# Performance work log

Hardware: AMD Instinct MI355X
Metric: run time of the kernel (lower is better)

Reference implementation:

```python
import jax, jax.numpy as jnp
import numpy as np
import math

N, D, BITS = 2048, 1024, 8
K = 1 << BITS          # 256 centroids
NG = (D + 1) // 2      # 512 rotation groups

def setup_inputs() -> dict:
    key = jax.random.key(0)
    kx, kc, kr = jax.random.split(key, 3)
    x = jax.random.normal(kx, (N, D), dtype=jnp.float32)
    # Lloyd-Max style scalar codebook: sorted centroids for a Gaussian source
    centroids = jnp.sort(jax.random.normal(kc, (K,), dtype=jnp.float32))
    # random planar rotations: [cos(theta), sin(theta)] per 2D group
    angles = jax.random.uniform(kr, (NG,), dtype=jnp.float32) * (2.0 * math.pi)
    rot2 = jnp.stack([jnp.cos(angles), jnp.sin(angles)], axis=-1)  # [NG, 2]
    return {"x": x, "centroids": centroids, "rot2": rot2}

def reference(x, centroids, rot2):
    d = x.shape[-1]
    n_groups = rot2.shape[0]
    d_padded = 2 * n_groups
    # unit-normalize rows
    norms = jnp.clip(jnp.linalg.norm(x, axis=-1, keepdims=True), 1e-8)  # [N,1]
    x_unit = x / norms
    pad = d_padded - d
    if pad > 0:
        x_unit = jnp.pad(x_unit, [(0, 0)] * (x.ndim - 1) + [(0, pad)])
    v = x_unit.reshape(*x.shape[:-1], n_groups, 2)                      # [N,NG,2]
    c, s = rot2[..., 0], rot2[..., 1]
    v0, v1 = v[..., 0], v[..., 1]
    v_rot = jnp.stack([c * v0 - s * v1, s * v0 + c * v1], axis=-1)      # rotate
    flat = v_rot.reshape(*v_rot.shape[:-2], -1)                         # [N,d_padded]
    # per-scalar nearest-centroid quantization
    indices = jnp.argmin(jnp.abs(flat[..., None] - centroids), axis=-1) # [N,d_padded]
    values = centroids[indices]
    v_q = values.reshape(*values.shape[:-1], n_groups, 2)
    q0, q1 = v_q[..., 0], v_q[..., 1]
    v_rec = jnp.stack([c * q0 + s * q1, -s * q0 + c * q1], axis=-1)     # inverse rotate
    x_hat = v_rec.reshape(*v_rec.shape[:-2], -1)[..., :d] * norms       # rescale
    return (x_hat, indices)
```

## Files before the change

kernel.cpp:

```cpp
#include <hip/hip_runtime.h>
#include <cfloat>

#define NROWS 2048
#define DDIM  1024
#define KCEN  256

__global__ __launch_bounds__(256)
void planar_quant_kernel(const float* __restrict__ x,
                         const float* __restrict__ cen,
                         const float* __restrict__ rot,
                         float* __restrict__ out_xhat,
                         float* __restrict__ out_idx)
{
    __shared__ float s_cen[KCEN];
    __shared__ float s_mid[KCEN];
    __shared__ float s_red[4];
    __shared__ float s_norm;

    const int row = blockIdx.x;
    const int t   = threadIdx.x;

    s_cen[t] = cen[t];
    __syncthreads();
    s_mid[t] = (t < KCEN - 1) ? 0.5f * (s_cen[t] + s_cen[t + 1]) : FLT_MAX;

    const float4 xv = *(const float4*)(x + (size_t)row * DDIM + 4 * t);
    const float4 rv = *(const float4*)(rot + 4 * t);

    float ss = xv.x * xv.x + xv.y * xv.y + xv.z * xv.z + xv.w * xv.w;
    #pragma unroll
    for (int off = 32; off >= 1; off >>= 1)
        ss += __shfl_xor(ss, off, 64);
    if ((t & 63) == 0) s_red[t >> 6] = ss;
    __syncthreads();
    if (t == 0) {
        float tot = s_red[0] + s_red[1] + s_red[2] + s_red[3];
        s_norm = fmaxf(sqrtf(tot), 1e-8f);
    }
    __syncthreads();
    const float nrm = s_norm;
    const float inv = 1.0f / nrm;

    float v0 = xv.x * inv, v1 = xv.y * inv, v2 = xv.z * inv, v3 = xv.w * inv;

    float r[4];
    r[0] = rv.x * v0 - rv.y * v1;
    r[1] = rv.y * v0 + rv.x * v1;
    r[2] = rv.z * v2 - rv.w * v3;
    r[3] = rv.w * v2 + rv.z * v3;

    int   qi[4];
    float qv[4];
    #pragma unroll
    for (int e = 0; e < 4; ++e) {
        const float v = r[e];
        int idx = 0;
        #pragma unroll
        for (int step = 128; step >= 1; step >>= 1) {
            if (s_mid[idx + step - 1] < v) idx += step;
        }
        float best = fabsf(v - s_cen[idx]);
        if (idx > 0 && fabsf(v - s_cen[idx - 1]) <= best) {
            idx -= 1;
        } else if (idx < KCEN - 1 && fabsf(v - s_cen[idx + 1]) < best) {
            idx += 1;
        }
        qi[e] = idx;
        qv[e] = s_cen[idx];
    }

    float4 xh;
    xh.x = ( rv.x * qv[0] + rv.y * qv[1]) * nrm;
    xh.y = (-rv.y * qv[0] + rv.x * qv[1]) * nrm;
    xh.z = ( rv.z * qv[2] + rv.w * qv[3]) * nrm;
    xh.w = (-rv.w * qv[2] + rv.z * qv[3]) * nrm;

    float4 fi;
    fi.x = (float)qi[0]; fi.y = (float)qi[1]; fi.z = (float)qi[2]; fi.w = (float)qi[3];

    const size_t off = (size_t)row * DDIM + 4 * t;
    *(float4*)(out_xhat + off) = xh;
    *(float4*)(out_idx  + off) = fi;
}

extern "C" void kernel_launch(void* const* d_in, const int* in_sizes, int n_in,
                              void* d_out, int out_size, void* d_ws, size_t ws_size,
                              hipStream_t stream) {
    const float* x   = (const float*)d_in[0];
    const float* cen = (const float*)d_in[1];
    const float* rot = (const float*)d_in[2];
    float* out       = (float*)d_out;

    planar_quant_kernel<<<NROWS, 256, 0, stream>>>(
        x, cen, rot, out, out + (size_t)NROWS * DDIM);
}
```

Baseline: 68.98 us.

## Replace binary search with uniform-bin lookup table plus linear fixup

Each block builds a 2048-entry shared-memory table that maps uniform bins over the midpoint range to a starting centroid index. Every value is then located with one table lookup and a short wave-uniform linear walk, in place of an 8-step dependent binary search. The code also drops one barrier by folding the centroid load into the norm-reduction barrier. The cost is building the table in every block, a data-dependent loop whose length depends on how centroids are spread, and extra shared-memory use.

```diff
diff --git a/kernel.cpp b/kernel.cpp
--- a/kernel.cpp
+++ b/kernel.cpp
@@ -4,6 +4,7 @@
 #define NROWS 2048
 #define DDIM  1024
 #define KCEN  256
+#define NBINS 2048
 
 __global__ __launch_bounds__(256)
 void planar_quant_kernel(const float* __restrict__ x,
@@ -14,59 +15,92 @@
 {
     __shared__ float s_cen[KCEN];
     __shared__ float s_mid[KCEN];
+    __shared__ unsigned short s_base[NBINS];
     __shared__ float s_red[4];
     __shared__ float s_norm;
 
     const int row = blockIdx.x;
     const int t   = threadIdx.x;
 
-    s_cen[t] = cen[t];
-    __syncthreads();
-    s_mid[t] = (t < KCEN - 1) ? 0.5f * (s_cen[t] + s_cen[t + 1]) : FLT_MAX;
-
     const float4 xv = *(const float4*)(x + (size_t)row * DDIM + 4 * t);
     const float4 rv = *(const float4*)(rot + 4 * t);
+    const float  cv = cen[t];
+
+    s_cen[t] = cv;
 
     float ss = xv.x * xv.x + xv.y * xv.y + xv.z * xv.z + xv.w * xv.w;
     #pragma unroll
     for (int off = 32; off >= 1; off >>= 1)
         ss += __shfl_xor(ss, off, 64);
     if ((t & 63) == 0) s_red[t >> 6] = ss;
+
     __syncthreads();
+
     if (t == 0) {
-        float tot = s_red[0] + s_red[1] + s_red[2] + s_red[3];
+        const float tot = s_red[0] + s_red[1] + s_red[2] + s_red[3];
         s_norm = fmaxf(sqrtf(tot), 1e-8f);
     }
+
+    const float lo    = 0.5f * (s_cen[0] + s_cen[1]);
+    const float hi    = 0.5f * (s_cen[KCEN - 2] + s_cen[KCEN - 1]);
+    const float invw  = (float)NBINS / fmaxf(hi - lo, 1e-30f);
+    const float nbm1f = (float)(NBINS - 1);
+
+#define BIN_OF(m) ((int)fminf(fmaxf(((m) - (lo)) * invw, 0.0f), nbm1f))
+
+    {
+        const float cm    = s_cen[(t > 0) ? (t - 1) : 0];
+        const float cp    = s_cen[(t < KCEN - 1) ? (t + 1) : (KCEN - 1)];
+        const float mid_c = (t < KCEN - 1) ? 0.5f * (cv + cp) : FLT_MAX;
+        s_mid[t] = mid_c;
+
+        const int jc = BIN_OF(mid_c);
+        const int jp = (t > 0) ? BIN_OF(0.5f * (cm + cv)) : -1;
+        for (int b = jp + 1; b <= jc; ++b)
+            s_base[b] = (unsigned short)t;
+    }
+
     __syncthreads();
+
     const float nrm = s_norm;
     const float inv = 1.0f / nrm;
 
-    float v0 = xv.x * inv, v1 = xv.y * inv, v2 = xv.z * inv, v3 = xv.w * inv;
+    const float v0 = xv.x * inv, v1 = xv.y * inv, v2 = xv.z * inv, v3 = xv.w * inv;
 
-    float r[4];
-    r[0] = rv.x * v0 - rv.y * v1;
-    r[1] = rv.y * v0 + rv.x * v1;
-    r[2] = rv.z * v2 - rv.w * v3;
-    r[3] = rv.w * v2 + rv.z * v3;
+    const float r0 = rv.x * v0 - rv.y * v1;
+    const float r1 = rv.y * v0 + rv.x * v1;
+    const float r2 = rv.z * v2 - rv.w * v3;
+    const float r3 = rv.w * v2 + rv.z * v3;
 
+    int i0 = s_base[BIN_OF(r0)];
+    int i1 = s_base[BIN_OF(r1)];
+    int i2 = s_base[BIN_OF(r2)];
+    int i3 = s_base[BIN_OF(r3)];
+
+    while (true) {
+        const float m0 = s_mid[i0], m1 = s_mid[i1], m2 = s_mid[i2], m3 = s_mid[i3];
+        const int c0 = m0 < r0, c1 = m1 < r1, c2 = m2 < r2, c3 = m3 < r3;
+        if (!__any(c0 | c1 | c2 | c3)) break;
+        i0 += c0; i1 += c1; i2 += c2; i3 += c3;
+    }
+
+    const int   ii[4] = {i0, i1, i2, i3};
+    const float rr[4] = {r0, r1, r2, r3};
     int   qi[4];
     float qv[4];
     #pragma unroll
     for (int e = 0; e < 4; ++e) {
-        const float v = r[e];
-        int idx = 0;
-        #pragma unroll
-        for (int step = 128; step >= 1; step >>= 1) {
-            if (s_mid[idx + step - 1] < v) idx += step;
-        }
-        float best = fabsf(v - s_cen[idx]);
-        if (idx > 0 && fabsf(v - s_cen[idx - 1]) <= best) {
-            idx -= 1;
-        } else if (idx < KCEN - 1 && fabsf(v - s_cen[idx + 1]) < best) {
-            idx += 1;
-        }
-        qi[e] = idx;
-        qv[e] = s_cen[idx];
+        const int   idx = ii[e];
+        const float v   = rr[e];
+        const int   im  = (idx > 0) ? idx - 1 : 0;
+        const int   ip  = (idx < KCEN - 1) ? idx + 1 : KCEN - 1;
+        const float cc  = s_cen[idx];
+        const float cl  = s_cen[im];
+        const float cr  = s_cen[ip];
+        const float best = fabsf(v - cc);
+        if (idx > 0 && fabsf(v - cl) <= best)            { qi[e] = im;  qv[e] = cl; }
+        else if (idx < KCEN - 1 && fabsf(v - cr) < best) { qi[e] = ip;  qv[e] = cr; }
+        else                                             { qi[e] = idx; qv[e] = cc; }
     }
 
     float4 xh;
@@ -81,6 +115,7 @@
     const size_t off = (size_t)row * DDIM + 4 * t;
     *(float4*)(out_xhat + off) = xh;
     *(float4*)(out_idx  + off) = fi;
+#undef BIN_OF
 }
 
 extern "C" void kernel_launch(void* const* d_in, const int* in_sizes, int n_in,
```

Result: slower. 71.39 us (+3.5%).
